# Kernel optimization log

Hardware: AMD Instinct MI355X
Metric: run time of the kernel (lower is better)

The kernel has to match this reference:

```python
import jax, jax.numpy as jnp
import numpy as np

# Hardware-emulation constants (from init_kwargs, NeuroSim-style QLinear)
WL_IN = 8        # input activation bit width (bit-serial)
WL_W = 8         # weight bit width
CELL_BIT = 2     # bits per memory cell -> 4 weight slices
SUB = 128        # crossbar sub-array size (rows summed in analog)
ADC_BITS = 5     # ADC precision per partial sum
ONOFF = 10.0     # cell on/off conductance ratio
VARI = 0.05      # multiplicative device variation sigma


def _adc_quant(x, bits, axes):
    # LinearQuantizeOut: uniform quantization between tensor min/max
    mn = jnp.min(x, axis=axes, keepdims=True)
    mx = jnp.max(x, axis=axes, keepdims=True)
    step = (mx - mn) * (2.0 ** (-bits))
    step = jnp.where(step <= 0, 1.0, step)
    idx = jnp.clip(jnp.floor((x - mn) / step), 0.0, 2.0 ** bits - 1.0)
    return idx * step + mn


def _qlinear_hw(x, w, noise):
    """Analog PIM crossbar emulation of y = x @ w.T with bit-serial inputs,
    bit-sliced cells, on/off-ratio offset + dummy column, device variation,
    per-subarray ADC quantization."""
    B, N = x.shape
    F = w.shape[0]
    I, W, K = WL_IN, WL_W, WL_W // CELL_BIT
    cr = 2.0 ** CELL_BIT
    lower, upper = 1.0 / ONOFF, 1.0
    S = (N + SUB - 1) // SUB
    Np = S * SUB
    # quantize input to I bits in [0,1]; weight to W-bit integer in [0, 2^W-1]
    xq = jnp.round(jnp.clip(x, 0.0, 1.0) * (2.0 ** I - 1.0))            # [B, N]
    Xi = jnp.clip(jnp.round((w + 1.0) * 0.5 * (2.0 ** W - 1.0)), 0.0, 2.0 ** W - 1.0)  # [F, N]
    xq = jnp.pad(xq, ((0, 0), (0, Np - N)))
    Xi = jnp.pad(Xi, ((0, 0), (0, Np - N)))
    zpow = 2.0 ** jnp.arange(I, dtype=x.dtype)
    kpow = cr ** jnp.arange(K, dtype=x.dtype)
    bits = jnp.mod(jnp.floor(xq[..., None] / zpow), 2.0)                # [B, Np, I]
    slc = jnp.mod(jnp.floor(Xi[..., None] / kpow), cr)                  # [F, Np, K]
    g = slc * (upper - lower) + (cr - 1.0) * lower                      # cell conductances
    g = g * (1.0 + VARI * noise)                                        # device variation
    bits = bits.reshape(B, S, SUB, I)
    g = g.reshape(F, S, SUB, K)
    # analog partial sums per (input bit i, subarray s, weight slice k)
    P = jnp.einsum('bsai,fsak->iskbf', bits, g)                         # [I,S,K,B,F]
    # dummy column (all cells at lowest conductance), identical across F
    D = jnp.transpose(bits.sum(axis=2), (2, 1, 0)) * ((cr - 1.0) * lower)  # [I,S,B]
    Pq = _adc_quant(P, ADC_BITS, axes=(3, 4))
    Dq = _adc_quant(D, ADC_BITS, axes=(2,))
    scal = (2.0 ** jnp.arange(I, dtype=x.dtype))[:, None] * (cr ** jnp.arange(K, dtype=x.dtype))[None, :]
    acc = jnp.einsum('iskbf,ik->bf', Pq - Dq[:, :, None, :, None], scal) / (upper - lower)
    # undo integer mappings: w = 2*Xi/(2^W-1) - 1, x = xq/(2^I-1)
    out = 2.0 * acc / ((2.0 ** I - 1.0) * (2.0 ** W - 1.0)) \
          - xq.sum(axis=1, keepdims=True) / (2.0 ** I - 1.0)
    return out


def _qlinear(x, w, noise):
    # straight-through quantized weight (WAGE-style STE) + hardware forward
    Xi = jnp.clip(jnp.round((w + 1.0) * 0.5 * (2.0 ** WL_W - 1.0)), 0.0, 2.0 ** WL_W - 1.0)
    wq = 2.0 * Xi / (2.0 ** WL_W - 1.0) - 1.0
    wq_ste = w + jax.lax.stop_gradient(wq - w)
    out_ideal = x @ wq_ste.T
    out_hw = _qlinear_hw(x, w, noise)
    return out_ideal + jax.lax.stop_gradient(out_hw - out_ideal)


def setup_inputs() -> dict:
    key = jax.random.key(0)
    k1, k2, k3, k4, k5 = jax.random.split(key, 5)
    x = jax.random.uniform(k1, (1024, 784), dtype=jnp.float32)
    w1 = jax.random.normal(k2, (512, 784), dtype=jnp.float32) * 0.05
    w3 = jax.random.normal(k3, (10, 512), dtype=jnp.float32) * 0.08
    noise1 = jax.random.normal(k4, (512, 896, 4), dtype=jnp.float32)  # 784 padded to 7*128
    noise3 = jax.random.normal(k5, (10, 512, 4), dtype=jnp.float32)   # 512 = 4*128 exact
    return {"x": x, "w1": w1, "w3": w3, "noise1": noise1, "noise3": noise3}


def reference(x, w1, w3, noise1, noise3):
    h = jnp.tanh(_qlinear(x, w1, noise1))   # QLinear(784,512) + Tanh
    return _qlinear(h, w3, noise3)          # QLinear(512,10)
```

## Files before the change

### kernel.cpp

```cpp
#include <hip/hip_runtime.h>

#define FLTMAX 3.402823466e+38f

typedef float f32x2 __attribute__((ext_vector_type(2)));


__device__ __forceinline__ void slot_barrier(unsigned* ctr, unsigned target)
{
    __syncthreads();
    if (threadIdx.x == 0) {
        asm volatile("s_waitcnt vmcnt(0)" ::: "memory");
        __hip_atomic_fetch_add(ctr, 1u, __ATOMIC_RELAXED, __HIP_MEMORY_SCOPE_AGENT);
        for (int it = 0; it < (1 << 22); ++it) {
            if (__hip_atomic_load(ctr, __ATOMIC_RELAXED, __HIP_MEMORY_SCOPE_AGENT) >= target)
                break;
            __builtin_amdgcn_s_sleep(2);
        }
    }
    __syncthreads();
}

__global__ void prep1_kernel(const float* __restrict__ x, float* __restrict__ sx1,
                             unsigned* __restrict__ xqbT, unsigned* __restrict__ stats1,
                             unsigned* __restrict__ bar)
{
    __shared__ float xr[896];
    __shared__ float red[128];
    int b = blockIdx.x;
    if (b == 0) {
        for (int t = threadIdx.x; t < 224; t += 128) {
            stats1[t * 2] = 0x7F7FFFFFu; stats1[t * 2 + 1] = 0u;
        }
        for (int t = threadIdx.x; t < 3584; t += 128) bar[t] = 0u;
    }
    float psum = 0.f;
    for (int n = threadIdx.x; n < 896; n += 128) {
        float v = 0.f;
        if (n < 784) {
            float xv = x[b * 784 + n];
            xv = fminf(fmaxf(xv, 0.f), 1.f);
            v = rintf(__fmul_rn(xv, 255.f));
        }
        xr[n] = v;
        psum += v;
    }
    red[threadIdx.x] = psum;
    __syncthreads();
    for (int w = 64; w >= 1; w >>= 1) {
        if (threadIdx.x < w) red[threadIdx.x] += red[threadIdx.x + w];
        __syncthreads();
    }
    if (threadIdx.x == 0) sx1[b] = red[0];
    if (threadIdx.x < 28) {
        int w = threadIdx.x;
        unsigned words[8] = {0, 0, 0, 0, 0, 0, 0, 0};
#pragma unroll 8
        for (int n = 0; n < 32; ++n) {
            int v = (int)xr[w * 32 + n];
#pragma unroll
            for (int i = 0; i < 8; ++i) words[i] |= ((unsigned)((v >> i) & 1)) << n;
        }
#pragma unroll
        for (int i = 0; i < 8; ++i) xqbT[(i * 28 + w) * 1024 + b] = words[i];
    }
}

__global__ void prepg1t_kernel(const float* __restrict__ w1, const float* __restrict__ noise1,
                               float* __restrict__ g1t)
{
    __shared__ float t[4][32][33];
    const int n0 = blockIdx.x * 32, f0 = blockIdx.y * 32;
    const int tid = threadIdx.x;
    {
        int n = tid & 31, fi = tid >> 5;
#pragma unroll
        for (int p = 0; p < 4; ++p) {
            int f = p * 8 + fi;
            int gn = n0 + n, gf = f0 + f;
            float gv[4] = {0.f, 0.f, 0.f, 0.f};
            if (gn < 784) {
                float w = w1[gf * 784 + gn];
                float Xi = fminf(fmaxf(rintf(__fmul_rn(__fmul_rn(__fadd_rn(w, 1.f), 0.5f), 255.f)),
                                       0.f), 255.f);
                int xi = (int)Xi;
                float4 nz = *(const float4*)&noise1[(gf * 896 + gn) * 4];
                float nzv[4] = {nz.x, nz.y, nz.z, nz.w};
#pragma unroll
                for (int k = 0; k < 4; ++k) {
                    int slc = (xi >> (2 * k)) & 3;
                    float base = __fadd_rn(__fmul_rn((float)slc, 0.9f), 0.3f);
                    float nf = __fadd_rn(1.f, __fmul_rn(0.05f, nzv[k]));
                    gv[k] = __fmul_rn(base, nf);
                }
            }
#pragma unroll
            for (int k = 0; k < 4; ++k) t[k][n][f] = gv[k];
        }
    }
    __syncthreads();
    {
        int f = tid & 31, nn = tid >> 5;
#pragma unroll
        for (int p = 0; p < 4; ++p) {
            int n = p * 8 + nn;
#pragma unroll
            for (int k = 0; k < 4; ++k)
                g1t[(n0 + n) * 2048 + k * 512 + f0 + f] = t[k][n][f];
        }
    }
}

__global__ void prepg2_kernel(const float* __restrict__ w3, const float* __restrict__ noise3,
                              float* __restrict__ g2t)
{
    int gid = blockIdx.x * 256 + threadIdx.x;
    if (gid >= 10 * 512) return;
    int f = gid / 512, n = gid % 512;
    float w = w3[f * 512 + n];
    float Xi = fminf(fmaxf(rintf(__fmul_rn(__fmul_rn(__fadd_rn(w, 1.f), 0.5f), 255.f)),
                           0.f), 255.f);
    int xi = (int)Xi;
#pragma unroll
    for (int k = 0; k < 4; ++k) {
        int slc = (xi >> (2 * k)) & 3;
        float base = __fadd_rn(__fmul_rn((float)slc, 0.9f), 0.3f);
        float nf = __fadd_rn(1.f, __fmul_rn(0.05f, noise3[(f * 512 + n) * 4 + k]));
        g2t[n * 40 + k * 10 + f] = __fmul_rn(base, nf);
    }
}

__global__ void dqpopT_kernel(const unsigned* __restrict__ xqbT, float* __restrict__ Dq)
{
    __shared__ float red[512];
    const int i = blockIdx.x / 7, s = blockIdx.x % 7;
    const int tid = threadIdx.x;
    float D[4];
    float mn = FLTMAX, mx = -FLTMAX;
#pragma unroll
    for (int u = 0; u < 4; ++u) {
        int b = tid + u * 256;
        int c = 0;
#pragma unroll
        for (int w = 0; w < 4; ++w)
            c += __popc(xqbT[(i * 28 + s * 4 + w) * 1024 + b]);
        D[u] = __fmul_rn((float)c, 0.3f);
        mn = fminf(mn, D[u]);
        mx = fmaxf(mx, D[u]);
    }
    red[tid] = mn; red[256 + tid] = mx;
    __syncthreads();
    for (int w = 128; w >= 1; w >>= 1) {
        if (tid < w) {
            red[tid] = fminf(red[tid], red[tid + w]);
            red[256 + tid] = fmaxf(red[256 + tid], red[256 + tid + w]);
        }
        __syncthreads();
    }
    mn = red[0]; mx = red[256];
    float step = __fmul_rn(__fsub_rn(mx, mn), 0.03125f);
    if (step <= 0.f) step = 1.f;
#pragma unroll
    for (int u = 0; u < 4; ++u) {
        int b = tid + u * 256;
        float idx = fminf(fmaxf(floorf(__fdiv_rn(__fsub_rn(D[u], mn), step)), 0.f), 31.f);
        Dq[(i * 7 + s) * 1024 + b] = __fadd_rn(__fmul_rn(idx, step), mn);
    }
}

__global__ void dqpop_kernel(const unsigned* __restrict__ xqb, float* __restrict__ Dq,
                             int S, int wpr)
{
    __shared__ float red[512];
    const int i = blockIdx.x / S, s = blockIdx.x % S;
    const int tid = threadIdx.x;
    float D[4];
    float mn = FLTMAX, mx = -FLTMAX;
#pragma unroll
    for (int u = 0; u < 4; ++u) {
        int b = tid + u * 256;
        uint4 w = *(const uint4*)&xqb[(i * 1024 + b) * wpr + s * 4];
        int c = __popc(w.x) + __popc(w.y) + __popc(w.z) + __popc(w.w);
        D[u] = __fmul_rn((float)c, 0.3f);
        mn = fminf(mn, D[u]);
        mx = fmaxf(mx, D[u]);
    }
    red[tid] = mn; red[256 + tid] = mx;
    __syncthreads();
    for (int w = 128; w >= 1; w >>= 1) {
        if (tid < w) {
            red[tid] = fminf(red[tid], red[tid + w]);
            red[256 + tid] = fmaxf(red[256 + tid], red[256 + tid + w]);
        }
        __syncthreads();
    }
    mn = red[0]; mx = red[256];
    float step = __fmul_rn(__fsub_rn(mx, mn), 0.03125f);
    if (step <= 0.f) step = 1.f;
#pragma unroll
    for (int u = 0; u < 4; ++u) {
        int b = tid + u * 256;
        float idx = fminf(fmaxf(floorf(__fdiv_rn(__fsub_rn(D[u], mn), step)), 0.f), 31.f);
        Dq[(i * S + s) * 1024 + b] = __fadd_rn(__fmul_rn(idx, step), mn);
    }
}

#define BK 32
__global__ __launch_bounds__(256, 2) void mm1_kernel(
    const unsigned* __restrict__ xqbT, const float* __restrict__ g1t,
    unsigned char* __restrict__ Pidx, unsigned* stats, unsigned* bar)
{
    __shared__ __align__(16) float Bs[BK][132];
    __shared__ unsigned Abits[256];
    __shared__ float red[512];
    __shared__ __align__(16) unsigned stage[2][128 * 33];
    const int tid = threadIdx.x;
    const int pair = blockIdx.x & 31;
    const int i = pair >> 2;
    const int bp = (pair & 3) * 256;
    const int btile0 = (pair * 2) & 7;
    const int colgrp = blockIdx.x >> 5;
    const int colBase = colgrp * 128;
    const int tx = tid & 15, ty = tid >> 4;
    const int aB = tid >> 5;
    const int eB = (tid & 31) << 2;
    const int k = colgrp >> 2;
    const int wv = tid >> 6, ln = tid & 63;
    const int rsub = ln >> 3, chunk = ln & 7;

    for (int s = 0; s < 7; ++s) {
        float4 pB[4];
#pragma unroll
        for (int u = 0; u < 4; ++u)
            pB[u] = *(const float4*)&g1t[(s * 128 + u * 8 + aB) * 2048 + colBase + eB];
        unsigned pAw = xqbT[(i * 28 + s * 4) * 1024 + bp + tid];

        f32x2 acc[2][8][4] = {};

        for (int ac = 0; ac < 4; ++ac) {
            __syncthreads();
#pragma unroll
            for (int u = 0; u < 4; ++u)
                *(float4*)&Bs[u * 8 + aB][eB] = pB[u];
            Abits[tid] = pAw;
            __syncthreads();

            if (ac < 3) {
                const int n0 = s * 128 + (ac + 1) * BK;
#pragma unroll
                for (int u = 0; u < 4; ++u)
                    pB[u] = *(const float4*)&g1t[(n0 + u * 8 + aB) * 2048 + colBase + eB];
                pAw = xqbT[(i * 28 + s * 4 + ac + 1) * 1024 + bp + tid];
            }

            unsigned wrd[2][8];
#pragma unroll
            for (int q = 0; q < 2; ++q)
#pragma unroll
                for (int u = 0; u < 4; ++u) {
                    wrd[q][u]     = Abits[q * 128 + (ty << 2) + u];
                    wrd[q][4 + u] = Abits[q * 128 + 64 + (ty << 2) + u];
                }

#pragma unroll 4
            for (int a = 0; a < BK; ++a) {
                float4 b0 = *(const float4*)&Bs[a][(tx << 2)];
                float4 b1 = *(const float4*)&Bs[a][64 + (tx << 2)];
                f32x2 br[4];
                br[0] = (f32x2){b0.x, b0.y}; br[1] = (f32x2){b0.z, b0.w};
                br[2] = (f32x2){b1.x, b1.y}; br[3] = (f32x2){b1.z, b1.w};
#pragma unroll
                for (int q = 0; q < 2; ++q)
#pragma unroll
                    for (int u = 0; u < 8; ++u) {
                        float ab = (float)((wrd[q][u] >> a) & 1u);
                        f32x2 abv = {ab, ab};
#pragma unroll
                        for (int p = 0; p < 4; ++p)
                            acc[q][u][p] = __builtin_elementwise_fma(abv, br[p], acc[q][u][p]);
                    }
            }
        }

        float mn = acc[0][0][0].x, mx = acc[0][0][0].x;
#pragma unroll
        for (int q = 0; q < 2; ++q)
#pragma unroll
            for (int u = 0; u < 8; ++u)
#pragma unroll
                for (int p = 0; p < 4; ++p) {
                    mn = fminf(mn, acc[q][u][p].x); mx = fmaxf(mx, acc[q][u][p].x);
                    mn = fminf(mn, acc[q][u][p].y); mx = fmaxf(mx, acc[q][u][p].y);
                }
        red[tid] = mn; red[256 + tid] = mx;
        __syncthreads();
        for (int w = 128; w >= 1; w >>= 1) {
            if (tid < w) {
                red[tid] = fminf(red[tid], red[tid + w]);
                red[256 + tid] = fmaxf(red[256 + tid], red[256 + tid + w]);
            }
            __syncthreads();
        }
        const int slot = ((s * 8 + i) * 4 + k);
        if (tid == 0) {
            atomicMin(&stats[slot * 2],     __float_as_uint(red[0]));
            atomicMax(&stats[slot * 2 + 1], __float_as_uint(red[256]));
        }

        slot_barrier(&bar[slot * 16], 16u);

        unsigned mnu = __hip_atomic_load(&stats[slot * 2],     __ATOMIC_RELAXED,
                                         __HIP_MEMORY_SCOPE_AGENT);
        unsigned mxu = __hip_atomic_load(&stats[slot * 2 + 1], __ATOMIC_RELAXED,
                                         __HIP_MEMORY_SCOPE_AGENT);
        float qmn = __uint_as_float(mnu);
        float qmx = __uint_as_float(mxu);
        float step = __fmul_rn(__fsub_rn(qmx, qmn), 0.03125f);
        if (step <= 0.f) step = 1.f;

#pragma unroll
        for (int q = 0; q < 2; ++q)
#pragma unroll
            for (int uh = 0; uh < 2; ++uh)
#pragma unroll
                for (int u = 0; u < 4; ++u) {
                    int rr = uh * 64 + (ty << 2) + u;
#pragma unroll
                    for (int vh = 0; vh < 2; ++vh) {
                        f32x2 e0 = acc[q][uh * 4 + u][vh * 2];
                        f32x2 e1 = acc[q][uh * 4 + u][vh * 2 + 1];
                        float ix;
                        unsigned pack;
                        ix = fminf(fmaxf(floorf(__fdiv_rn(__fsub_rn(e0.x, qmn), step)), 0.f), 31.f);
                        pack = (unsigned)(int)ix;
                        ix = fminf(fmaxf(floorf(__fdiv_rn(__fsub_rn(e0.y, qmn), step)), 0.f), 31.f);
                        pack |= (unsigned)(int)ix << 8;
                        ix = fminf(fmaxf(floorf(__fdiv_rn(__fsub_rn(e1.x, qmn), step)), 0.f), 31.f);
                        pack |= (unsigned)(int)ix << 16;
                        ix = fminf(fmaxf(floorf(__fdiv_rn(__fsub_rn(e1.y, qmn), step)), 0.f), 31.f);
                        pack |= (unsigned)(int)ix << 24;
                        stage[q][rr * 33 + vh * 16 + tx] = pack;
                    }
                }
        __syncthreads();

#pragma unroll
        for (int q = 0; q < 2; ++q) {
            unsigned char* tbase = Pidx +
                ((size_t)(((s * 8 + i) * 16 + colgrp) * 8 + btile0 + q)) * 16384;
#pragma unroll
            for (int t = 0; t < 4; ++t) {
                int rr = t * 32 + wv * 8 + rsub;
                const unsigned* sp = &stage[q][rr * 33 + chunk * 4];
                uint4 v = make_uint4(sp[0], sp[1], sp[2], sp[3]);
                *(uint4*)&tbase[rr * 128 + chunk * 16] = v;
            }
        }
        __syncthreads();
    }
}

__global__ void fold1_kernel(const unsigned char* __restrict__ Pidx,
                             const unsigned* __restrict__ stats,
                             const float* __restrict__ Dq1, const float* __restrict__ sx1,
                             float* __restrict__ xq2, unsigned* __restrict__ xqb2,
                             float* __restrict__ sx2)
{
    __shared__ float red[512];
    __shared__ float dt;
    __shared__ float2 st[224];
    int b = blockIdx.x;
    int f = threadIdx.x;
    if (f < 224) {
        float mn = __uint_as_float(stats[f * 2]);
        float mx = __uint_as_float(stats[f * 2 + 1]);
        float step = __fmul_rn(__fsub_rn(mx, mn), 0.03125f);
        if (step <= 0.f) step = 1.f;
        st[f] = make_float2(mn, step);
    }
    if (f == 0) {
        float sd = 0.f;
        for (int i = 0; i < 8; ++i) {
            float sc = (float)(85 << i);
            for (int ss = 0; ss < 7; ++ss) sd = fmaf(Dq1[(i * 7 + ss) * 1024 + b], sc, sd);
        }
        dt = sd;
    }
    __syncthreads();
    const int fhi = f >> 7, fl = f & 127;
    const unsigned char* pb = Pidx + (size_t)(b >> 7) * 16384
                                   + (size_t)(b & 127) * 128 + fl;
    float accR = 0.f;
    for (int s = 0; s < 7; ++s) {
        float sum = 0.f;
        for (int i = 0; i < 8; ++i) {
            const int si16 = (s * 8 + i) * 16;
#pragma unroll
            for (int kk = 0; kk < 4; ++kk) {
                float2 ms = st[((s * 8 + i) << 2) + kk];
                float ixv = (float)pb[(size_t)(si16 + kk * 4 + fhi) * 131072];
                float pq = __fadd_rn(__fmul_rn(ixv, ms.y), ms.x);
                sum = fmaf(pq, (float)(1 << (i + 2 * kk)), sum);
            }
        }
        accR = __fadd_rn(accR, sum);
    }
    float total = __fsub_rn(accR, dt);
    float acc = __fdiv_rn(total, 0.9f);
    float o = __fsub_rn(__fdiv_rn(__fmul_rn(2.f, acc), 65025.f), __fdiv_rn(sx1[b], 255.f));
    float h = tanhf(o);
    h = fminf(fmaxf(h, 0.f), 1.f);
    float code = rintf(__fmul_rn(h, 255.f));
    xq2[b * 512 + f] = code;
    int ci = (int)code;
    int lane = f & 63;
#pragma unroll
    for (int i = 0; i < 8; ++i) {
        unsigned long long m = __ballot((ci >> i) & 1);
        if ((lane & 31) == 0) {
            unsigned wv = (lane & 32) ? (unsigned)(m >> 32) : (unsigned)m;
            xqb2[(i * 1024 + b) * 16 + (f >> 5)] = wv;
        }
    }
    red[f] = code;
    __syncthreads();
    for (int w = 256; w >= 1; w >>= 1) {
        if (f < w) red[f] += red[f + w];
        __syncthreads();
    }
    if (f == 0) sx2[b] = red[0];
}

__global__ void mm2_kernel(const float* __restrict__ xq2, const float* __restrict__ g2t,
                           float* __restrict__ P2)
{
    int gid = blockIdx.x * 256 + threadIdx.x;
    if (gid >= 40960) return;
    int f = gid % 10;
    int b = (gid / 10) & 1023;
    int s = gid / 10240;
    float acc[8][4] = {};
    for (int a = 0; a < 128; ++a) {
        int n = s * 128 + a;
        int xi = (int)xq2[b * 512 + n];
        float g0 = g2t[n * 40 + f];
        float gA = g2t[n * 40 + 10 + f];
        float gB = g2t[n * 40 + 20 + f];
        float gC = g2t[n * 40 + 30 + f];
#pragma unroll
        for (int i = 0; i < 8; ++i) {
            float bi = (float)((xi >> i) & 1);
            acc[i][0] = fmaf(bi, g0, acc[i][0]);
            acc[i][1] = fmaf(bi, gA, acc[i][1]);
            acc[i][2] = fmaf(bi, gB, acc[i][2]);
            acc[i][3] = fmaf(bi, gC, acc[i][3]);
        }
    }
#pragma unroll
    for (int i = 0; i < 8; ++i)
#pragma unroll
        for (int k = 0; k < 4; ++k)
            P2[(size_t)((s * 8 + i) * 4 + k) * 10240 + b * 10 + f] = acc[i][k];
}

__global__ void stat2_kernel(const float* __restrict__ P2, float2* __restrict__ stats2)
{
    __shared__ float red[512];
    int p = blockIdx.x;
    int tid = threadIdx.x;
    float mn = FLTMAX, mx = -FLTMAX;
    for (int t = tid; t < 10240; t += 256) {
        float v = P2[(size_t)p * 10240 + t];
        mn = fminf(mn, v); mx = fmaxf(mx, v);
    }
    red[tid] = mn; red[256 + tid] = mx;
    __syncthreads();
    for (int w = 128; w >= 1; w >>= 1) {
        if (tid < w) {
            red[tid] = fminf(red[tid], red[tid + w]);
            red[256 + tid] = fmaxf(red[256 + tid], red[256 + tid + w]);
        }
        __syncthreads();
    }
    if (tid == 0) {
        float step = __fmul_rn(__fsub_rn(red[256], red[0]), 0.03125f);
        if (step <= 0.f) step = 1.f;
        stats2[p] = make_float2(red[0], step);
    }
}

__global__ void out2_kernel(const float* __restrict__ P2, const float2* __restrict__ stats2,
                            const float* __restrict__ Dq2, const float* __restrict__ sx2,
                            float* __restrict__ out)
{
    int gid = blockIdx.x * 256 + threadIdx.x;
    if (gid >= 10240) return;
    int b = gid / 10;
    float dt = 0.f;
    for (int i = 0; i < 8; ++i) {
        float sc = (float)(85 << i);
        for (int s = 0; s < 4; ++s) dt = fmaf(Dq2[(i * 4 + s) * 1024 + b], sc, dt);
    }
    float sum = 0.f;
    for (int s = 0; s < 4; ++s)
        for (int i = 0; i < 8; ++i)
#pragma unroll
            for (int k = 0; k < 4; ++k) {
                int p = (s * 8 + i) * 4 + k;
                float2 st = stats2[p];
                float val = P2[(size_t)p * 10240 + gid];
                float idx = fminf(fmaxf(floorf(__fdiv_rn(__fsub_rn(val, st.x), st.y)), 0.f), 31.f);
                float pq = __fadd_rn(__fmul_rn(idx, st.y), st.x);
                sum = fmaf(pq, (float)(1 << (i + 2 * k)), sum);
            }
    float total = __fsub_rn(sum, dt);
    float acc = __fdiv_rn(total, 0.9f);
    out[gid] = __fsub_rn(__fdiv_rn(__fmul_rn(2.f, acc), 65025.f), __fdiv_rn(sx2[b], 255.f));
}

extern "C" void kernel_launch(void* const* d_in, const int* in_sizes, int n_in,
                              void* d_out, int out_size, void* d_ws, size_t ws_size,
                              hipStream_t stream)
{
    const float* x      = (const float*)d_in[0];
    const float* w1     = (const float*)d_in[1];
    const float* w3     = (const float*)d_in[2];
    const float* noise1 = (const float*)d_in[3];
    const float* noise3 = (const float*)d_in[4];
    float* out = (float*)d_out;
    float* ws  = (float*)d_ws;

    float*         g1t    = ws + 0;
    float*         xq2    = ws + 1835008;
    float*         P2     = ws + 2359296;
    float*         g2t    = ws + 3670016;
    float*         Dq1    = ws + 3690496;
    float*         Dq2    = ws + 3747840;
    float*         sx1    = ws + 3780608;
    float*         sx2    = ws + 3781632;
    float2*        stats2 = (float2*)(ws + 3782656);
    unsigned*      stats1 = (unsigned*)(ws + 3782912);
    unsigned*      xqbT   = (unsigned*)(ws + 3783424);
    unsigned*      xqb2   = (unsigned*)(ws + 4012800);
    unsigned char* Pidx   = (unsigned char*)(ws + 4143872);
    unsigned*      bar    = (unsigned*)(ws + 33504256);

    prep1_kernel<<<1024, 128, 0, stream>>>(x, sx1, xqbT, stats1, bar);
    prepg1t_kernel<<<dim3(28, 16), 256, 0, stream>>>(w1, noise1, g1t);
    dqpopT_kernel<<<56, 256, 0, stream>>>(xqbT, Dq1);

    mm1_kernel<<<512, 256, 0, stream>>>(xqbT, g1t, Pidx, stats1, bar);

    fold1_kernel<<<1024, 512, 0, stream>>>(Pidx, stats1, Dq1, sx1, xq2, xqb2, sx2);
    prepg2_kernel<<<20, 256, 0, stream>>>(w3, noise3, g2t);
    dqpop_kernel<<<32, 256, 0, stream>>>(xqb2, Dq2, 4, 16);
    mm2_kernel<<<160, 256, 0, stream>>>(xq2, g2t, P2);
    stat2_kernel<<<128, 256, 0, stream>>>(P2, stats2);
    out2_kernel<<<40, 256, 0, stream>>>(P2, stats2, Dq2, sx2, out);
}
```

Measured before the change: 624.6 us.

## Double mm1 block size to 512 threads with halved per-thread tile

```diff
diff --git a/kernel.cpp b/kernel.cpp
--- a/kernel.cpp
+++ b/kernel.cpp
@@ -205,61 +205,57 @@
 }
 
 #define BK 32
-__global__ __launch_bounds__(256, 2) void mm1_kernel(
+__global__ __launch_bounds__(512, 4) void mm1_kernel(
     const unsigned* __restrict__ xqbT, const float* __restrict__ g1t,
     unsigned char* __restrict__ Pidx, unsigned* stats, unsigned* bar)
 {
     __shared__ __align__(16) float Bs[BK][132];
     __shared__ unsigned Abits[256];
-    __shared__ float red[512];
+    __shared__ float red[1024];
     __shared__ __align__(16) unsigned stage[2][128 * 33];
     const int tid = threadIdx.x;
     const int pair = blockIdx.x & 31;
     const int i = pair >> 2;
     const int bp = (pair & 3) * 256;
-    const int btile0 = (pair * 2) & 7;
+    const int btile0 = (pair & 3) * 2;
     const int colgrp = blockIdx.x >> 5;
     const int colBase = colgrp * 128;
     const int tx = tid & 15, ty = tid >> 4;
     const int aB = tid >> 5;
     const int eB = (tid & 31) << 2;
     const int k = colgrp >> 2;
-    const int wv = tid >> 6, ln = tid & 63;
-    const int rsub = ln >> 3, chunk = ln & 7;
 
     for (int s = 0; s < 7; ++s) {
-        float4 pB[4];
-#pragma unroll
-        for (int u = 0; u < 4; ++u)
-            pB[u] = *(const float4*)&g1t[(s * 128 + u * 8 + aB) * 2048 + colBase + eB];
-        unsigned pAw = xqbT[(i * 28 + s * 4) * 1024 + bp + tid];
-
-        f32x2 acc[2][8][4] = {};
+        float4 pB[2];
+#pragma unroll
+        for (int u = 0; u < 2; ++u)
+            pB[u] = *(const float4*)&g1t[(s * 128 + u * 16 + aB) * 2048 + colBase + eB];
+        unsigned pAw = (tid < 256) ? xqbT[(i * 28 + s * 4) * 1024 + bp + tid] : 0u;
+
+        f32x2 acc[2][4][4] = {};
 
         for (int ac = 0; ac < 4; ++ac) {
             __syncthreads();
 #pragma unroll
-            for (int u = 0; u < 4; ++u)
-                *(float4*)&Bs[u * 8 + aB][eB] = pB[u];
-            Abits[tid] = pAw;
+            for (int u = 0; u < 2; ++u)
+                *(float4*)&Bs[u * 16 + aB][eB] = pB[u];
+            if (tid < 256) Abits[tid] = pAw;
             __syncthreads();
 
             if (ac < 3) {
                 const int n0 = s * 128 + (ac + 1) * BK;
 #pragma unroll
+                for (int u = 0; u < 2; ++u)
+                    pB[u] = *(const float4*)&g1t[(n0 + u * 16 + aB) * 2048 + colBase + eB];
+                if (tid < 256) pAw = xqbT[(i * 28 + s * 4 + ac + 1) * 1024 + bp + tid];
+            }
+
+            unsigned wrd[2][4];
+#pragma unroll
+            for (int q = 0; q < 2; ++q)
+#pragma unroll
                 for (int u = 0; u < 4; ++u)
-                    pB[u] = *(const float4*)&g1t[(n0 + u * 8 + aB) * 2048 + colBase + eB];
-                pAw = xqbT[(i * 28 + s * 4 + ac + 1) * 1024 + bp + tid];
-            }
-
-            unsigned wrd[2][8];
-#pragma unroll
-            for (int q = 0; q < 2; ++q)
-#pragma unroll
-                for (int u = 0; u < 4; ++u) {
-                    wrd[q][u]     = Abits[q * 128 + (ty << 2) + u];
-                    wrd[q][4 + u] = Abits[q * 128 + 64 + (ty << 2) + u];
-                }
+                    wrd[q][u] = Abits[q * 128 + (ty << 2) + u];
 
 #pragma unroll 4
             for (int a = 0; a < BK; ++a) {
@@ -271,7 +267,7 @@
 #pragma unroll
                 for (int q = 0; q < 2; ++q)
 #pragma unroll
-                    for (int u = 0; u < 8; ++u) {
+                    for (int u = 0; u < 4; ++u) {
                         float ab = (float)((wrd[q][u] >> a) & 1u);
                         f32x2 abv = {ab, ab};
 #pragma unroll
@@ -285,25 +281,25 @@
 #pragma unroll
         for (int q = 0; q < 2; ++q)
 #pragma unroll
-            for (int u = 0; u < 8; ++u)
+            for (int u = 0; u < 4; ++u)
 #pragma unroll
                 for (int p = 0; p < 4; ++p) {
                     mn = fminf(mn, acc[q][u][p].x); mx = fmaxf(mx, acc[q][u][p].x);
                     mn = fminf(mn, acc[q][u][p].y); mx = fmaxf(mx, acc[q][u][p].y);
                 }
-        red[tid] = mn; red[256 + tid] = mx;
-        __syncthreads();
-        for (int w = 128; w >= 1; w >>= 1) {
+        red[tid] = mn; red[512 + tid] = mx;
+        __syncthreads();
+        for (int w = 256; w >= 1; w >>= 1) {
             if (tid < w) {
                 red[tid] = fminf(red[tid], red[tid + w]);
-                red[256 + tid] = fmaxf(red[256 + tid], red[256 + tid + w]);
+                red[512 + tid] = fmaxf(red[512 + tid], red[512 + tid + w]);
             }
             __syncthreads();
         }
         const int slot = ((s * 8 + i) * 4 + k);
         if (tid == 0) {
             atomicMin(&stats[slot * 2],     __float_as_uint(red[0]));
-            atomicMax(&stats[slot * 2 + 1], __float_as_uint(red[256]));
+            atomicMax(&stats[slot * 2 + 1], __float_as_uint(red[512]));
         }
 
         slot_barrier(&bar[slot * 16], 16u);
@@ -320,27 +316,25 @@
 #pragma unroll
         for (int q = 0; q < 2; ++q)
 #pragma unroll
-            for (int uh = 0; uh < 2; ++uh)
-#pragma unroll
-                for (int u = 0; u < 4; ++u) {
-                    int rr = uh * 64 + (ty << 2) + u;
-#pragma unroll
-                    for (int vh = 0; vh < 2; ++vh) {
-                        f32x2 e0 = acc[q][uh * 4 + u][vh * 2];
-                        f32x2 e1 = acc[q][uh * 4 + u][vh * 2 + 1];
-                        float ix;
-                        unsigned pack;
-                        ix = fminf(fmaxf(floorf(__fdiv_rn(__fsub_rn(e0.x, qmn), step)), 0.f), 31.f);
-                        pack = (unsigned)(int)ix;
-                        ix = fminf(fmaxf(floorf(__fdiv_rn(__fsub_rn(e0.y, qmn), step)), 0.f), 31.f);
-                        pack |= (unsigned)(int)ix << 8;
-                        ix = fminf(fmaxf(floorf(__fdiv_rn(__fsub_rn(e1.x, qmn), step)), 0.f), 31.f);
-                        pack |= (unsigned)(int)ix << 16;
-                        ix = fminf(fmaxf(floorf(__fdiv_rn(__fsub_rn(e1.y, qmn), step)), 0.f), 31.f);
-                        pack |= (unsigned)(int)ix << 24;
-                        stage[q][rr * 33 + vh * 16 + tx] = pack;
-                    }
+            for (int u = 0; u < 4; ++u) {
+                int rr = (ty << 2) + u;
+#pragma unroll
+                for (int vh = 0; vh < 2; ++vh) {
+                    f32x2 e0 = acc[q][u][vh * 2];
+                    f32x2 e1 = acc[q][u][vh * 2 + 1];
+                    float ix;
+                    unsigned pack;
+                    ix = fminf(fmaxf(floorf(__fdiv_rn(__fsub_rn(e0.x, qmn), step)), 0.f), 31.f);
+                    pack = (unsigned)(int)ix;
+                    ix = fminf(fmaxf(floorf(__fdiv_rn(__fsub_rn(e0.y, qmn), step)), 0.f), 31.f);
+                    pack |= (unsigned)(int)ix << 8;
+                    ix = fminf(fmaxf(floorf(__fdiv_rn(__fsub_rn(e1.x, qmn), step)), 0.f), 31.f);
+                    pack |= (unsigned)(int)ix << 16;
+                    ix = fminf(fmaxf(floorf(__fdiv_rn(__fsub_rn(e1.y, qmn), step)), 0.f), 31.f);
+                    pack |= (unsigned)(int)ix << 24;
+                    stage[q][rr * 33 + vh * 16 + tx] = pack;
                 }
+            }
         __syncthreads();
 
 #pragma unroll
@@ -348,11 +342,12 @@
             unsigned char* tbase = Pidx +
                 ((size_t)(((s * 8 + i) * 16 + colgrp) * 8 + btile0 + q)) * 16384;
 #pragma unroll
-            for (int t = 0; t < 4; ++t) {
-                int rr = t * 32 + wv * 8 + rsub;
-                const unsigned* sp = &stage[q][rr * 33 + chunk * 4];
+            for (int rep = 0; rep < 2; ++rep) {
+                int j = rep * 512 + tid;
+                int rr = j >> 3, c4 = (j & 7) << 2;
+                const unsigned* sp = &stage[q][rr * 33 + c4];
                 uint4 v = make_uint4(sp[0], sp[1], sp[2], sp[3]);
-                *(uint4*)&tbase[rr * 128 + chunk * 16] = v;
+                *(uint4*)&tbase[(size_t)j * 16] = v;
             }
         }
         __syncthreads();
@@ -548,7 +543,7 @@
     prepg1t_kernel<<<dim3(28, 16), 256, 0, stream>>>(w1, noise1, g1t);
     dqpopT_kernel<<<56, 256, 0, stream>>>(xqbT, Dq1);
 
-    mm1_kernel<<<512, 256, 0, stream>>>(xqbT, g1t, Pidx, stats1, bar);
+    mm1_kernel<<<512, 512, 0, stream>>>(xqbT, g1t, Pidx, stats1, bar);
 
     fold1_kernel<<<1024, 512, 0, stream>>>(Pidx, stats1, Dq1, sx1, xq2, xqb2, sx2);
     prepg2_kernel<<<20, 256, 0, stream>>>(w3, noise3, g2t);
```

Result: slower. 640.9 us (+2.6%).
